# Optimization experiments

Hardware: AMD Instinct MI355X
Metric: run time of the kernel (lower is better)

## Reference

```python
import jax, jax.numpy as jnp
import numpy as np

N, E, G = 50000, 800000, 64
D_IN, D_H, D_OUT = 128, 256, 128
NEG_SLOPE = 0.01
BN_EPS = 1e-5


def setup_inputs() -> dict:
    key = jax.random.key(0)
    ks = jax.random.split(key, 20)
    x = jax.random.normal(ks[0], (N, D_IN), dtype=jnp.float32)
    edge_index = jax.random.randint(ks[1], (2, E), 0, N, dtype=jnp.int64)
    batch = jnp.sort(jax.random.randint(ks[2], (N,), 0, G, dtype=jnp.int64))
    dims = [(D_IN, D_H), (D_H, D_H), (D_H, D_H), (D_H, D_OUT)]
    inp = {"x": x, "edge_index": edge_index, "batch": batch}
    for i, (di, do) in enumerate(dims, start=1):
        s = 1.0 / np.sqrt(di)
        inp[f"W{i}"] = jax.random.normal(ks[3 + 4 * i], (di, do), dtype=jnp.float32) * s
        inp[f"b{i}"] = jnp.zeros((do,), dtype=jnp.float32)
        inp[f"g{i}"] = jnp.ones((do,), dtype=jnp.float32)
        inp[f"bt{i}"] = jnp.zeros((do,), dtype=jnp.float32)
    return inp


def _gcn_block(h, src, dst, norm, self_norm, W, b, g, bt):
    # GCNConv: h' = D^-1/2 (A+I) D^-1/2 (h W) + b  (degrees include self-loops)
    h = h @ W                                                    # [N, do]
    agg = jax.ops.segment_sum(h[src] * norm[:, None], dst, num_segments=N)
    h = agg + h * self_norm[:, None] + b
    # LeakyReLU then BatchNorm (batch statistics, as in training-mode BN)
    h = jnp.where(h > 0, h, NEG_SLOPE * h)
    mu = h.mean(axis=0)
    var = ((h - mu) ** 2).mean(axis=0)
    return (h - mu) * jax.lax.rsqrt(var + BN_EPS) * g + bt


def reference(x, edge_index, batch, W1, b1, g1, bt1, W2, b2, g2, bt2,
              W3, b3, g3, bt3, W4, b4, g4, bt4):
    src, dst = edge_index[0], edge_index[1]
    deg = jax.ops.segment_sum(jnp.ones((E,), x.dtype), dst, num_segments=N) + 1.0
    dinv = jax.lax.rsqrt(deg)                 # [N]
    norm = dinv[src] * dinv[dst]              # [E] edge normalization
    self_norm = 1.0 / deg                     # [N] self-loop normalization
    h = _gcn_block(x, src, dst, norm, self_norm, W1, b1, g1, bt1)
    h = _gcn_block(h, src, dst, norm, self_norm, W2, b2, g2, bt2)
    h = _gcn_block(h, src, dst, norm, self_norm, W3, b3, g3, bt3)
    h = _gcn_block(h, src, dst, norm, self_norm, W4, b4, g4, bt4)
    # global mean pool over graphs
    counts = jax.ops.segment_sum(jnp.ones((N,), h.dtype), batch, num_segments=G)
    sums = jax.ops.segment_sum(h, batch, num_segments=G)
    return sums / jnp.maximum(counts, 1.0)[:, None]   # [G, D_OUT]
```

## Files before the change

kernel.cpp:

```cpp
#include <hip/hip_runtime.h>
#include <hip/hip_bf16.h>

#define NEG_SLOPE 0.01f
#define BN_EPS 1e-5f
#define POOL_S 16

typedef __attribute__((ext_vector_type(8))) short short8;
typedef __attribute__((ext_vector_type(4))) float f32x4;

__device__ __forceinline__ float bf2f(unsigned short b) {
    unsigned int u = ((unsigned int)b) << 16;
    float f; __builtin_memcpy(&f, &u, 4); return f;
}
__device__ __forceinline__ unsigned short f2bf(float f) {
    unsigned int u; __builtin_memcpy(&u, &f, 4);
    u = (u + 0x7FFFu + ((u >> 16) & 1u)) >> 16;
    return (unsigned short)u;
}

__device__ __forceinline__ void gload_lds16(const void* g, void* l) {
    __builtin_amdgcn_global_load_lds(
        (const __attribute__((address_space(1))) void*)g,
        (__attribute__((address_space(3))) void*)l, 16, 0, 0);
}

__global__ void k_cvt(const float* __restrict__ x, const float* __restrict__ dinv,
                      unsigned short* __restrict__ xb, int total8) {
    int i = blockIdx.x * blockDim.x + threadIdx.x;
    if (i < total8) {
        float dn = dinv[i >> 4];
        float4 a = ((const float4*)x)[i * 2];
        float4 b = ((const float4*)x)[i * 2 + 1];
        short8 o;
        o[0] = (short)f2bf(dn * a.x); o[1] = (short)f2bf(dn * a.y);
        o[2] = (short)f2bf(dn * a.z); o[3] = (short)f2bf(dn * a.w);
        o[4] = (short)f2bf(dn * b.x); o[5] = (short)f2bf(dn * b.y);
        o[6] = (short)f2bf(dn * b.z); o[7] = (short)f2bf(dn * b.w);
        ((short8*)xb)[i] = o;
    }
}

__global__ void k_count(const int* __restrict__ ei, int* __restrict__ cnt,
                        int* __restrict__ perm, int E) {
    int e0 = (blockIdx.x * blockDim.x + threadIdx.x) * 4;
    if (e0 + 3 < E) {
        int4 d = *(const int4*)(ei + E + e0);
        int4 pv;
        pv.x = atomicAdd(&cnt[d.x], 1);
        pv.y = atomicAdd(&cnt[d.y], 1);
        pv.z = atomicAdd(&cnt[d.z], 1);
        pv.w = atomicAdd(&cnt[d.w], 1);
        *(int4*)(perm + e0) = pv;
    } else {
        for (int e = e0; e < E; ++e) perm[e] = atomicAdd(&cnt[ei[E + e]], 1);
    }
}

__global__ __launch_bounds__(256) void k_scan1(const int* __restrict__ cnt,
                                               int* __restrict__ bsum,
                                               float* __restrict__ dinv, int n) {
    int b = blockIdx.x;
    int t = threadIdx.x;
    if (b == 0 && t == 0) dinv[n] = 0.f;
    int base = b * 1024 + t * 4;
    int s = 0;
    #pragma unroll
    for (int i = 0; i < 4; ++i) {
        if (base + i < n) {
            int v = cnt[base + i];
            dinv[base + i] = rsqrtf((float)(v + 1));
            s += (v + 3) & ~3;
        }
    }
    #pragma unroll
    for (int off = 1; off < 64; off <<= 1) s += __shfl_xor(s, off, 64);
    __shared__ int ws[4];
    if ((t & 63) == 0) ws[t >> 6] = s;
    __syncthreads();
    if (t == 0) bsum[b] = ws[0] + ws[1] + ws[2] + ws[3];
}

__global__ void k_scan2(const int* __restrict__ bsum, int* __restrict__ boff,
                        int* __restrict__ row_ptr, int nb, int n) {
    int lane = threadIdx.x;
    int v = (lane < nb) ? bsum[lane] : 0;
    int x = v;
    #pragma unroll
    for (int off = 1; off < 64; off <<= 1) {
        int t = __shfl_up(x, off, 64);
        if (lane >= off) x += t;
    }
    if (lane < nb) boff[lane] = x - v;
    if (lane == 63) row_ptr[n] = x;
}

__global__ __launch_bounds__(256) void k_scan3(const int* __restrict__ cnt,
                                               const int* __restrict__ boff,
                                               int* __restrict__ row_ptr,
                                               int* __restrict__ eidx, int n) {
    int b = blockIdx.x;
    int t = threadIdx.x;
    int lane = t & 63, w = t >> 6;
    int base = b * 1024 + t * 4;
    int orig[4], v[4];
    #pragma unroll
    for (int i = 0; i < 4; ++i) {
        orig[i] = (base + i < n) ? cnt[base + i] : 0;
        v[i] = (orig[i] + 3) & ~3;
    }
    int tsum = v[0] + v[1] + v[2] + v[3];
    int x = tsum;
    #pragma unroll
    for (int off = 1; off < 64; off <<= 1) {
        int tt = __shfl_up(x, off, 64);
        if (lane >= off) x += tt;
    }
    __shared__ int ws[4];
    if (lane == 63) ws[w] = x;
    __syncthreads();
    int woff = 0;
    for (int k = 0; k < 4; ++k) if (k < w) woff += ws[k];
    int excl = boff[b] + woff + x - tsum;
    #pragma unroll
    for (int i = 0; i < 4; ++i) {
        if (base + i < n) {
            row_ptr[base + i] = excl;
            for (int j = excl + orig[i]; j < excl + v[i]; ++j) eidx[j] = n;
        }
        excl += v[i];
    }
}

__global__ void k_fill(const int* __restrict__ ei, const int* __restrict__ row_ptr,
                       const int* __restrict__ perm, int* __restrict__ eidx, int E) {
    int e0 = (blockIdx.x * blockDim.x + threadIdx.x) * 4;
    if (e0 + 3 < E) {
        int4 s = *(const int4*)(ei + e0);
        int4 d = *(const int4*)(ei + E + e0);
        int4 pv = *(const int4*)(perm + e0);
        eidx[row_ptr[d.x] + pv.x] = s.x;
        eidx[row_ptr[d.y] + pv.y] = s.y;
        eidx[row_ptr[d.z] + pv.z] = s.z;
        eidx[row_ptr[d.w] + pv.w] = s.w;
    } else {
        for (int e = e0; e < E; ++e)
            eidx[row_ptr[ei[E + e]] + perm[e]] = ei[e];
    }
}

__global__ void k_zero(unsigned short* __restrict__ xb, unsigned short* __restrict__ bufA,
                       unsigned short* __restrict__ bufB, int N) {
    int t = threadIdx.x;
    if (t < 128) xb[(size_t)N * 128 + t] = 0;
    if (t < 128) bufA[(size_t)N * 128 + t] = 0;
    bufB[(size_t)N * 256 + t] = 0;
}

__global__ void k_zeroA128(unsigned short* __restrict__ bufA, int N) {
    int t = threadIdx.x;
    bufA[(size_t)N * 128 + t] = 0;
}

__global__ __launch_bounds__(256) void k_ssum(const int* __restrict__ row_ptr,
                                              const int* __restrict__ eidx,
                                              const float* __restrict__ dinv,
                                              float* __restrict__ S, int N) {
    int n = blockIdx.x * 4 + (threadIdx.x >> 6);
    if (n >= N) return;
    int l = threadIdx.x & 63;
    int b = row_ptr[n], e = row_ptr[n + 1];
    float s = 0.f;
    for (int j = b + l * 4; j < e; j += 256) {
        int4 sv = *(const int4*)(eidx + j);
        s += (dinv[sv.x] + dinv[sv.y]) + (dinv[sv.z] + dinv[sv.w]);
    }
    #pragma unroll
    for (int off = 1; off < 64; off <<= 1) s += __shfl_xor(s, off, 64);
    if (l == 0) S[n] = s;
}

__global__ void k_init_affine(float* __restrict__ s, float* __restrict__ sh,
                              float* __restrict__ sums) {
    int c = threadIdx.x;
    s[c] = 1.0f;
    sh[c] = 0.0f;
    sums[c] = 0.f;
    sums[256 + c] = 0.f;
}

__global__ void k_prepW(const float* __restrict__ W, const float* __restrict__ scale,
                        unsigned short* __restrict__ Wt, int K, int DO) {
    int idx = blockIdx.x * blockDim.x + threadIdx.x;
    if (idx < K * DO) {
        int k = idx / DO, n = idx % DO;
        float v = W[idx];
        if (scale) v *= scale[k];
        Wt[(size_t)n * K + k] = f2bf(v);
    }
}

__global__ __launch_bounds__(256) void k_prepd(const float* __restrict__ W,
                                               const float* __restrict__ sh,
                                               float* __restrict__ d, int K, int DO) {
    int c = blockIdx.x;
    int t = threadIdx.x;
    float a = (t < K) ? sh[t] * W[(size_t)t * DO + c] : 0.f;
    #pragma unroll
    for (int off = 1; off < 64; off <<= 1) a += __shfl_xor(a, off, 64);
    __shared__ float ws[4];
    if ((t & 63) == 0) ws[t >> 6] = a;
    __syncthreads();
    if (t == 0) d[c] = ws[0] + ws[1] + ws[2] + ws[3];
}

template<int COLS, bool EPI>
__global__ __launch_bounds__(256) void k_aggw(const unsigned short* __restrict__ h,
    const float* __restrict__ s, const float* __restrict__ sh,
    const float* __restrict__ dv, const float* __restrict__ bias,
    const int* __restrict__ row_ptr, const int* __restrict__ eidx,
    const float* __restrict__ dinv, const float* __restrict__ S,
    unsigned short* __restrict__ t, int N) {
    constexpr int LPR = COLS / 8;
    constexpr int GR  = 64 / LPR;
    constexpr int SH  = (COLS == 256) ? 8 : 7;
    int n = blockIdx.x * 4 + (threadIdx.x >> 6);
    if (n >= N) return;
    int l = threadIdx.x & 63;
    int ct = l & (LPR - 1);
    int gp = l / LPR;
    const unsigned short* up = h + ct * 8;
    int b = row_ptr[n], e = row_ptr[n + 1];
    int cnt4 = e - b;
    int per = (((cnt4 + GR - 1) / GR) + 3) & ~3;
    int jb = b + gp * per;
    int je = min(jb + per, e);
    float acc[8] = {};
    if (gp == 0) {
        short8 hv = *(const short8*)(up + ((size_t)n << SH));
        #pragma unroll
        for (int i = 0; i < 8; ++i) acc[i] += bf2f((unsigned short)hv[i]);
    }
    for (int j = jb; j < je; j += 4) {
        int4 sv = *(const int4*)(eidx + j);
        short8 r0 = *(const short8*)(up + ((size_t)sv.x << SH));
        short8 r1 = *(const short8*)(up + ((size_t)sv.y << SH));
        short8 r2 = *(const short8*)(up + ((size_t)sv.z << SH));
        short8 r3 = *(const short8*)(up + ((size_t)sv.w << SH));
        #pragma unroll
        for (int i = 0; i < 8; ++i) {
            float a01 = bf2f((unsigned short)r0[i]) + bf2f((unsigned short)r1[i]);
            float a23 = bf2f((unsigned short)r2[i]) + bf2f((unsigned short)r3[i]);
            acc[i] += a01 + a23;
        }
    }
    #pragma unroll
    for (int mask = LPR; mask < 64; mask <<= 1) {
        #pragma unroll
        for (int i = 0; i < 8; ++i) acc[i] += __shfl_xor(acc[i], mask, 64);
    }
    if (gp == 0) {
        float dn = dinv[n];
        float ws = dn * S[n] + dn * dn;
        short8 ov;
        #pragma unroll
        for (int i = 0; i < 8; ++i) {
            int col = ct * 8 + i;
            float o;
            if constexpr (EPI) {
                o = dn * acc[i] + ws * dv[col] + bias[col];
                o = o > 0.f ? o : NEG_SLOPE * o;
            } else {
                o = s[col] * (dn * acc[i]) + sh[col] * ws;
            }
            ov[i] = (short)f2bf(o);
        }
        *(short8*)(t + ((size_t)n << SH) + ct * 8) = ov;
    }
}

template<int K, int DO, bool FUSE>
__global__ __launch_bounds__(256) void k_mfma2(
    const unsigned short* __restrict__ A, const unsigned short* __restrict__ Wt,
    const float* __restrict__ bias, const float* __restrict__ dinv,
    unsigned short* __restrict__ H, float* __restrict__ sums, int M) {
    __shared__ unsigned short Asm[128 * 64];
    __shared__ unsigned short Bsm[128 * 64];
    __shared__ float ls[2][128];
    int tid = threadIdx.x;
    int l = tid & 63, w = tid >> 6;
    int wr = w & 1, wc = w >> 1;
    int rl = l & 15, kh = l >> 4;
    int Rb = blockIdx.x * 128;
    int Cb = blockIdx.y * 128;
    int srow = tid >> 3;
    int sd   = tid & 7;
    f32x4 acc[4][4] = {};
    for (int k0 = 0; k0 < K; k0 += 64) {
        #pragma unroll
        for (int i = 0; i < 4; ++i) {
            int row = i * 32 + srow;
            int ss = sd ^ (row & 7);
            int rg = Rb + row; if (rg >= M) rg = M - 1;
            gload_lds16(A + (size_t)rg * K + k0 + ss * 8,
                        (char*)Asm + i * 4096 + w * 1024);
            gload_lds16(Wt + (size_t)(Cb + row) * K + k0 + ss * 8,
                        (char*)Bsm + i * 4096 + w * 1024);
        }
        __syncthreads();
        #pragma unroll
        for (int kk = 0; kk < 2; ++kk) {
            short8 af[4], bf[4];
            #pragma unroll
            for (int mf = 0; mf < 4; ++mf) {
                int r = wr * 64 + mf * 16 + rl;
                int slot = (kk * 4 + kh) ^ (r & 7);
                af[mf] = *(const short8*)((const char*)Asm + r * 128 + slot * 16);
            }
            #pragma unroll
            for (int nf = 0; nf < 4; ++nf) {
                int c = wc * 64 + nf * 16 + rl;
                int slot = (kk * 4 + kh) ^ (c & 7);
                bf[nf] = *(const short8*)((const char*)Bsm + c * 128 + slot * 16);
            }
            #pragma unroll
            for (int mf = 0; mf < 4; ++mf)
                #pragma unroll
                for (int nf = 0; nf < 4; ++nf)
                    acc[mf][nf] = __builtin_amdgcn_mfma_f32_16x16x32_bf16(
                        af[mf], bf[nf], acc[mf][nf], 0, 0, 0);
        }
        __syncthreads();
    }
    if constexpr (FUSE) {
        for (int c = tid; c < 128; c += 256) { ls[0][c] = 0.f; ls[1][c] = 0.f; }
        __syncthreads();
        float p1[4] = {}, p2[4] = {};
        #pragma unroll
        for (int mf = 0; mf < 4; ++mf) {
            #pragma unroll
            for (int r = 0; r < 4; ++r) {
                int row = Rb + wr * 64 + mf * 16 + kh * 4 + r;
                if (row < M) {
                    float dr = dinv[row];
                    #pragma unroll
                    for (int nf = 0; nf < 4; ++nf) {
                        int col = Cb + wc * 64 + nf * 16 + rl;
                        float z = acc[mf][nf][r] + bias[col];
                        z = z > 0.f ? z : NEG_SLOPE * z;
                        H[(size_t)row * DO + col] = f2bf(dr * z);
                        p1[nf] += z; p2[nf] += z * z;
                    }
                }
            }
        }
        #pragma unroll
        for (int nf = 0; nf < 4; ++nf) {
            int cl = wc * 64 + nf * 16 + rl;
            atomicAdd(&ls[0][cl], p1[nf]);
            atomicAdd(&ls[1][cl], p2[nf]);
        }
        __syncthreads();
        for (int c = tid; c < 128; c += 256) {
            atomicAdd(&sums[Cb + c], ls[0][c]);
            atomicAdd(&sums[256 + Cb + c], ls[1][c]);
        }
    } else {
        #pragma unroll
        for (int nf = 0; nf < 4; ++nf) {
            int col = Cb + wc * 64 + nf * 16 + rl;
            #pragma unroll
            for (int mf = 0; mf < 4; ++mf) {
                #pragma unroll
                for (int r = 0; r < 4; ++r) {
                    int row = Rb + wr * 64 + mf * 16 + kh * 4 + r;
                    if (row < M) H[(size_t)row * DO + col] = f2bf(acc[mf][nf][r]);
                }
            }
        }
    }
}

__global__ void k_finalize(float* __restrict__ sums, const float* __restrict__ g,
                           const float* __restrict__ bt, float* __restrict__ s_out,
                           float* __restrict__ sh_out, float Nf) {
    int c = threadIdx.x;
    float mu = sums[c] / Nf;
    float var = sums[256 + c] / Nf - mu * mu;
    float rs = rsqrtf(var + BN_EPS);
    float sc = g[c] * rs;
    s_out[c] = sc;
    sh_out[c] = bt[c] - mu * sc;
    sums[c] = 0.f;
    sums[256 + c] = 0.f;
}

__global__ void k_pool1(const unsigned short* __restrict__ h, const int* __restrict__ batch,
                        float* __restrict__ part, float* __restrict__ sums, int N) {
    int g = blockIdx.x;
    int sidx = blockIdx.y;
    int c = threadIdx.x;
    int lo = 0, hi = N;
    while (lo < hi) { int m = (lo + hi) >> 1; if (batch[m] < g) lo = m + 1; else hi = m; }
    int start = lo; hi = N;
    while (lo < hi) { int m = (lo + hi) >> 1; if (batch[m] < g + 1) lo = m + 1; else hi = m; }
    int end = lo;
    float acc = 0.f, sq = 0.f;
    for (int r = start + sidx; r < end; r += POOL_S) {
        float v = bf2f(h[(size_t)r * 128 + c]);
        acc += v; sq += v * v;
    }
    part[((size_t)g * POOL_S + sidx) * 128 + c] = acc;
    atomicAdd(&sums[c], acc);
    atomicAdd(&sums[256 + c], sq);
}

__global__ void k_pool2(const float* __restrict__ part, const int* __restrict__ batch,
                        const float* __restrict__ s, const float* __restrict__ sh,
                        float* __restrict__ out, int N) {
    int g = blockIdx.x;
    int c = threadIdx.x;
    int lo = 0, hi = N;
    while (lo < hi) { int m = (lo + hi) >> 1; if (batch[m] < g) lo = m + 1; else hi = m; }
    int start = lo; hi = N;
    while (lo < hi) { int m = (lo + hi) >> 1; if (batch[m] < g + 1) lo = m + 1; else hi = m; }
    int cnt = lo - start;
    float acc = 0.f;
    #pragma unroll
    for (int i = 0; i < POOL_S; ++i) acc += part[((size_t)g * POOL_S + i) * 128 + c];
    out[(size_t)g * 128 + c] = (cnt > 0) ? (s[c] * acc / (float)cnt + sh[c]) : 0.f;
}


static inline size_t align256(size_t x) { return (x + 255) & ~(size_t)255; }

extern "C" void kernel_launch(void* const* d_in, const int* in_sizes, int n_in,
                              void* d_out, int out_size, void* d_ws, size_t ws_size,
                              hipStream_t stream) {
    const float* x   = (const float*)d_in[0];
    const int* ei    = (const int*)d_in[1];
    const int* batch = (const int*)d_in[2];
    const float* Wp[4]  = {(const float*)d_in[3], (const float*)d_in[7],
                           (const float*)d_in[11], (const float*)d_in[15]};
    const float* bp[4]  = {(const float*)d_in[4], (const float*)d_in[8],
                           (const float*)d_in[12], (const float*)d_in[16]};
    const float* gp[4]  = {(const float*)d_in[5], (const float*)d_in[9],
                           (const float*)d_in[13], (const float*)d_in[17]};
    const float* btp[4] = {(const float*)d_in[6], (const float*)d_in[10],
                           (const float*)d_in[14], (const float*)d_in[18]};

    const int N = in_sizes[0] / 128;
    const int E = in_sizes[1] / 2;
    const int G = out_size / 128;

    char* p = (char*)d_ws;
    int* deg_cnt = (int*)p;            p += align256((size_t)N * 4);
    int* row_ptr = (int*)p;            p += align256((size_t)(N + 1) * 4);
    float* dinv = (float*)p;           p += align256((size_t)(N + 1) * 4);
    float* Svec = (float*)p;           p += align256((size_t)N * 4);
    int* bsum = (int*)p;               p += align256(64 * 4);
    int* boff = (int*)p;               p += align256(64 * 4);
    int* perm = (int*)p;               p += align256((size_t)E * 4);
    int* eidx = (int*)p;               p += align256((size_t)(E + 3 * (N + 1)) * 4);
    float* sums = (float*)p;           p += align256(512 * 4);
    float* s_arr = (float*)p;          p += align256(5 * 256 * 4);
    float* sh_arr = (float*)p;         p += align256(5 * 256 * 4);
    float* dvec = (float*)p;           p += align256(256 * 4);
    unsigned short* Wt = (unsigned short*)p; p += align256(256 * 256 * 2);
    float* part = (float*)p;           p += align256((size_t)G * POOL_S * 128 * 4);
    unsigned short* xb = (unsigned short*)p;   p += align256((size_t)(N + 1) * 128 * 2);
    unsigned short* bufA = (unsigned short*)p; p += align256((size_t)(N + 1) * 256 * 2);
    unsigned short* bufB = (unsigned short*)p; p += align256((size_t)(N + 1) * 256 * 2);

    hipMemsetAsync(deg_cnt, 0, (size_t)N * 4, stream);
    k_count<<<(E / 4 + 255) / 256, 256, 0, stream>>>(ei, deg_cnt, perm, E);
    const int nb = (N + 1023) / 1024;
    k_scan1<<<nb, 256, 0, stream>>>(deg_cnt, bsum, dinv, N);
    k_scan2<<<1, 64, 0, stream>>>(bsum, boff, row_ptr, nb, N);
    k_scan3<<<nb, 256, 0, stream>>>(deg_cnt, boff, row_ptr, eidx, N);
    k_fill<<<(E / 4 + 255) / 256, 256, 0, stream>>>(ei, row_ptr, perm, eidx, E);
    k_zero<<<1, 256, 0, stream>>>(xb, bufA, bufB, N);
    k_ssum<<<(N + 3) / 4, 256, 0, stream>>>(row_ptr, eidx, dinv, Svec, N);
    k_cvt<<<(N * 128 / 8 + 255) / 256, 256, 0, stream>>>(x, dinv, xb, N * 128 / 8);
    k_init_affine<<<1, 256, 0, stream>>>(s_arr, sh_arr, sums);

    const int ablocks = (N + 3) / 4;
    const int gx = (N + 127) / 128;

    k_aggw<128, false><<<ablocks, 256, 0, stream>>>(xb, s_arr, sh_arr, nullptr, nullptr,
        row_ptr, eidx, dinv, Svec, bufA, N);
    k_prepW<<<(128 * 256 + 255) / 256, 256, 0, stream>>>(Wp[0], nullptr, Wt, 128, 256);
    k_mfma2<128, 256, true><<<dim3(gx, 2), 256, 0, stream>>>(bufA, Wt, bp[0], dinv, bufB, sums, N);
    k_finalize<<<1, 256, 0, stream>>>(sums, gp[0], btp[0], s_arr + 256, sh_arr + 256, (float)N);

    for (int L = 1; L <= 2; ++L) {
        k_aggw<256, false><<<ablocks, 256, 0, stream>>>(bufB, s_arr + L * 256, sh_arr + L * 256,
            nullptr, nullptr, row_ptr, eidx, dinv, Svec, bufA, N);
        k_prepW<<<(256 * 256 + 255) / 256, 256, 0, stream>>>(Wp[L], nullptr, Wt, 256, 256);
        k_mfma2<256, 256, true><<<dim3(gx, 2), 256, 0, stream>>>(bufA, Wt, bp[L], dinv, bufB, sums, N);
        k_finalize<<<1, 256, 0, stream>>>(sums, gp[L], btp[L],
                                          s_arr + (L + 1) * 256, sh_arr + (L + 1) * 256, (float)N);
    }

    k_zeroA128<<<1, 128, 0, stream>>>(bufA, N);

    k_prepW<<<(256 * 128 + 255) / 256, 256, 0, stream>>>(Wp[3], s_arr + 3 * 256, Wt, 256, 128);
    k_prepd<<<128, 256, 0, stream>>>(Wp[3], sh_arr + 3 * 256, dvec, 256, 128);
    k_mfma2<256, 128, false><<<dim3(gx, 1), 256, 0, stream>>>(bufB, Wt, nullptr, dinv, bufA, nullptr, N);
    k_aggw<128, true><<<ablocks, 256, 0, stream>>>(bufA, nullptr, nullptr, dvec, bp[3],
        row_ptr, eidx, dinv, Svec, bufB, N);
    dim3 pgrid(G, POOL_S);
    k_pool1<<<pgrid, 128, 0, stream>>>(bufB, batch, part, sums, N);
    k_finalize<<<1, 128, 0, stream>>>(sums, gp[3], btp[3], s_arr + 4 * 256, sh_arr + 4 * 256, (float)N);
    k_pool2<<<G, 128, 0, stream>>>(part, batch, s_arr + 4 * 256, sh_arr + 4 * 256,
                                   (float*)d_out, N);
}
```

Baseline: 450.0 us.

## Merge tiny init kernels, enlarge aggregation blocks, prefetch edge indices

```diff
diff --git a/kernel.cpp b/kernel.cpp
--- a/kernel.cpp
+++ b/kernel.cpp
@@ -148,24 +148,24 @@
     }
 }
 
-__global__ void k_zero(unsigned short* __restrict__ xb, unsigned short* __restrict__ bufA,
+__global__ void k_init(float* __restrict__ s, float* __restrict__ sh,
+                       float* __restrict__ sums, unsigned short* __restrict__ xb,
+                       unsigned short* __restrict__ bufA,
                        unsigned short* __restrict__ bufB, int N) {
-    int t = threadIdx.x;
-    if (t < 128) xb[(size_t)N * 128 + t] = 0;
-    if (t < 128) bufA[(size_t)N * 128 + t] = 0;
-    bufB[(size_t)N * 256 + t] = 0;
-}
-
-__global__ void k_zeroA128(unsigned short* __restrict__ bufA, int N) {
-    int t = threadIdx.x;
-    bufA[(size_t)N * 128 + t] = 0;
-}
-
-__global__ __launch_bounds__(256) void k_ssum(const int* __restrict__ row_ptr,
+    int c = threadIdx.x;
+    s[c] = 1.0f;
+    sh[c] = 0.0f;
+    sums[c] = 0.f;
+    sums[256 + c] = 0.f;
+    if (c < 128) { xb[(size_t)N * 128 + c] = 0; bufA[(size_t)N * 128 + c] = 0; }
+    bufB[(size_t)N * 256 + c] = 0;
+}
+
+__global__ __launch_bounds__(512) void k_ssum(const int* __restrict__ row_ptr,
                                               const int* __restrict__ eidx,
                                               const float* __restrict__ dinv,
                                               float* __restrict__ S, int N) {
-    int n = blockIdx.x * 4 + (threadIdx.x >> 6);
+    int n = blockIdx.x * 8 + (threadIdx.x >> 6);
     if (n >= N) return;
     int l = threadIdx.x & 63;
     int b = row_ptr[n], e = row_ptr[n + 1];
@@ -177,15 +177,6 @@
     #pragma unroll
     for (int off = 1; off < 64; off <<= 1) s += __shfl_xor(s, off, 64);
     if (l == 0) S[n] = s;
-}
-
-__global__ void k_init_affine(float* __restrict__ s, float* __restrict__ sh,
-                              float* __restrict__ sums) {
-    int c = threadIdx.x;
-    s[c] = 1.0f;
-    sh[c] = 0.0f;
-    sums[c] = 0.f;
-    sums[256 + c] = 0.f;
 }
 
 __global__ void k_prepW(const float* __restrict__ W, const float* __restrict__ scale,
@@ -201,9 +192,12 @@
 
 __global__ __launch_bounds__(256) void k_prepd(const float* __restrict__ W,
                                                const float* __restrict__ sh,
-                                               float* __restrict__ d, int K, int DO) {
+                                               float* __restrict__ d,
+                                               unsigned short* __restrict__ bufA,
+                                               int K, int DO, int N) {
     int c = blockIdx.x;
     int t = threadIdx.x;
+    if (c == 0 && t < 128) bufA[(size_t)N * 128 + t] = 0;
     float a = (t < K) ? sh[t] * W[(size_t)t * DO + c] : 0.f;
     #pragma unroll
     for (int off = 1; off < 64; off <<= 1) a += __shfl_xor(a, off, 64);
@@ -214,7 +208,7 @@
 }
 
 template<int COLS, bool EPI>
-__global__ __launch_bounds__(256) void k_aggw(const unsigned short* __restrict__ h,
+__global__ __launch_bounds__(512) void k_aggw(const unsigned short* __restrict__ h,
     const float* __restrict__ s, const float* __restrict__ sh,
     const float* __restrict__ dv, const float* __restrict__ bias,
     const int* __restrict__ row_ptr, const int* __restrict__ eidx,
@@ -223,7 +217,7 @@
     constexpr int LPR = COLS / 8;
     constexpr int GR  = 64 / LPR;
     constexpr int SH  = (COLS == 256) ? 8 : 7;
-    int n = blockIdx.x * 4 + (threadIdx.x >> 6);
+    int n = blockIdx.x * 8 + (threadIdx.x >> 6);
     if (n >= N) return;
     int l = threadIdx.x & 63;
     int ct = l & (LPR - 1);
@@ -240,17 +234,22 @@
         #pragma unroll
         for (int i = 0; i < 8; ++i) acc[i] += bf2f((unsigned short)hv[i]);
     }
-    for (int j = jb; j < je; j += 4) {
-        int4 sv = *(const int4*)(eidx + j);
-        short8 r0 = *(const short8*)(up + ((size_t)sv.x << SH));
-        short8 r1 = *(const short8*)(up + ((size_t)sv.y << SH));
-        short8 r2 = *(const short8*)(up + ((size_t)sv.z << SH));
-        short8 r3 = *(const short8*)(up + ((size_t)sv.w << SH));
-        #pragma unroll
-        for (int i = 0; i < 8; ++i) {
-            float a01 = bf2f((unsigned short)r0[i]) + bf2f((unsigned short)r1[i]);
-            float a23 = bf2f((unsigned short)r2[i]) + bf2f((unsigned short)r3[i]);
-            acc[i] += a01 + a23;
+    if (jb < je) {
+        int4 sv = *(const int4*)(eidx + jb);
+        for (int j = jb; j < je; ) {
+            int4 cur = sv;
+            j += 4;
+            if (j < je) sv = *(const int4*)(eidx + j);
+            short8 r0 = *(const short8*)(up + ((size_t)cur.x << SH));
+            short8 r1 = *(const short8*)(up + ((size_t)cur.y << SH));
+            short8 r2 = *(const short8*)(up + ((size_t)cur.z << SH));
+            short8 r3 = *(const short8*)(up + ((size_t)cur.w << SH));
+            #pragma unroll
+            for (int i = 0; i < 8; ++i) {
+                float a01 = bf2f((unsigned short)r0[i]) + bf2f((unsigned short)r1[i]);
+                float a23 = bf2f((unsigned short)r2[i]) + bf2f((unsigned short)r3[i]);
+                acc[i] += a01 + a23;
+            }
         }
     }
     #pragma unroll
@@ -478,22 +477,21 @@
     k_scan2<<<1, 64, 0, stream>>>(bsum, boff, row_ptr, nb, N);
     k_scan3<<<nb, 256, 0, stream>>>(deg_cnt, boff, row_ptr, eidx, N);
     k_fill<<<(E / 4 + 255) / 256, 256, 0, stream>>>(ei, row_ptr, perm, eidx, E);
-    k_zero<<<1, 256, 0, stream>>>(xb, bufA, bufB, N);
-    k_ssum<<<(N + 3) / 4, 256, 0, stream>>>(row_ptr, eidx, dinv, Svec, N);
+    k_init<<<1, 256, 0, stream>>>(s_arr, sh_arr, sums, xb, bufA, bufB, N);
+    k_ssum<<<(N + 7) / 8, 512, 0, stream>>>(row_ptr, eidx, dinv, Svec, N);
     k_cvt<<<(N * 128 / 8 + 255) / 256, 256, 0, stream>>>(x, dinv, xb, N * 128 / 8);
-    k_init_affine<<<1, 256, 0, stream>>>(s_arr, sh_arr, sums);
-
-    const int ablocks = (N + 3) / 4;
+
+    const int ablocks = (N + 7) / 8;
     const int gx = (N + 127) / 128;
 
-    k_aggw<128, false><<<ablocks, 256, 0, stream>>>(xb, s_arr, sh_arr, nullptr, nullptr,
+    k_aggw<128, false><<<ablocks, 512, 0, stream>>>(xb, s_arr, sh_arr, nullptr, nullptr,
         row_ptr, eidx, dinv, Svec, bufA, N);
     k_prepW<<<(128 * 256 + 255) / 256, 256, 0, stream>>>(Wp[0], nullptr, Wt, 128, 256);
     k_mfma2<128, 256, true><<<dim3(gx, 2), 256, 0, stream>>>(bufA, Wt, bp[0], dinv, bufB, sums, N);
     k_finalize<<<1, 256, 0, stream>>>(sums, gp[0], btp[0], s_arr + 256, sh_arr + 256, (float)N);
 
     for (int L = 1; L <= 2; ++L) {
-        k_aggw<256, false><<<ablocks, 256, 0, stream>>>(bufB, s_arr + L * 256, sh_arr + L * 256,
+        k_aggw<256, false><<<ablocks, 512, 0, stream>>>(bufB, s_arr + L * 256, sh_arr + L * 256,
             nullptr, nullptr, row_ptr, eidx, dinv, Svec, bufA, N);
         k_prepW<<<(256 * 256 + 255) / 256, 256, 0, stream>>>(Wp[L], nullptr, Wt, 256, 256);
         k_mfma2<256, 256, true><<<dim3(gx, 2), 256, 0, stream>>>(bufA, Wt, bp[L], dinv, bufB, sums, N);
@@ -501,12 +499,10 @@
                                           s_arr + (L + 1) * 256, sh_arr + (L + 1) * 256, (float)N);
     }
 
-    k_zeroA128<<<1, 128, 0, stream>>>(bufA, N);
-
     k_prepW<<<(256 * 128 + 255) / 256, 256, 0, stream>>>(Wp[3], s_arr + 3 * 256, Wt, 256, 128);
-    k_prepd<<<128, 256, 0, stream>>>(Wp[3], sh_arr + 3 * 256, dvec, 256, 128);
+    k_prepd<<<128, 256, 0, stream>>>(Wp[3], sh_arr + 3 * 256, dvec, bufA, 256, 128, N);
     k_mfma2<256, 128, false><<<dim3(gx, 1), 256, 0, stream>>>(bufB, Wt, nullptr, dinv, bufA, nullptr, N);
-    k_aggw<128, true><<<ablocks, 256, 0, stream>>>(bufA, nullptr, nullptr, dvec, bp[3],
+    k_aggw<128, true><<<ablocks, 512, 0, stream>>>(bufA, nullptr, nullptr, dvec, bp[3],
         row_ptr, eidx, dinv, Svec, bufB, N);
     dim3 pgrid(G, POOL_S);
     k_pool1<<<pgrid, 128, 0, stream>>>(bufB, batch, part, sums, N);
```

New measurement: 445.8 us. Within noise of the previous version (-0.9%).
